# Optimization experiments

Measured on AMD Instinct MI355X. Metric: run time of the kernel, lower is better.

Reference implementation:

```python
import jax, jax.numpy as jnp
import numpy as np

S = 128          # spatial grid size per axis
N = 100000       # active voxels
C_IN = 32
C_OUT = 32
FS = 3           # filter size per axis -> 27 offsets


def _build_rulebook():
    """Build submanifold-conv rulebook: for each active site and each of the
    27 filter offsets, the index of the active neighbor (or masked out)."""
    rng = np.random.default_rng(0)
    coords = rng.integers(0, S, size=(2 * N, 3))
    lin = coords[:, 0] * S * S + coords[:, 1] * S + coords[:, 2]
    lin = np.unique(lin)[:N]                      # sorted unique active sites
    xyz = np.stack([lin // (S * S), (lin // S) % S, lin % S], axis=1)  # [N,3]
    offs = np.stack(np.meshgrid(*([np.arange(FS) - FS // 2] * 3), indexing='ij'), -1).reshape(-1, 3)  # [27,3]
    nb = xyz[:, None, :] + offs[None, :, :]       # [N,27,3]
    inb = np.all((nb >= 0) & (nb < S), axis=-1)   # in-bounds
    nb_lin = nb[..., 0] * S * S + nb[..., 1] * S + nb[..., 2]
    pos = np.searchsorted(lin, nb_lin)
    pos_c = np.clip(pos, 0, N - 1)
    found = inb & (lin[pos_c] == nb_lin)
    nbr_idx = np.where(found, pos_c, 0).astype(np.int32)   # [N,27]
    return nbr_idx, found


def setup_inputs() -> dict:
    key = jax.random.key(0)
    k1, k2 = jax.random.split(key)
    nbr_idx, nbr_mask = _build_rulebook()
    K = FS ** 3
    std = (2.0 / C_IN / K) ** 0.5   # matches module init
    return {
        'features': jax.random.normal(k1, (N, C_IN), dtype=jnp.float32),
        'weight': std * jax.random.normal(k2, (K, C_IN, C_OUT), dtype=jnp.float32),
        'bias': jnp.zeros((C_OUT,), dtype=jnp.float32),
        'nbr_idx': jnp.asarray(nbr_idx),
        'nbr_mask': jnp.asarray(nbr_mask),
    }


def reference(features, weight, bias, nbr_idx, nbr_mask):
    # Submanifold sparse conv: gather active neighbors per filter offset,
    # multiply by per-offset [Cin,Cout] weight, accumulate at active sites.
    gathered = jnp.where(nbr_mask[:, :, None], features[nbr_idx], 0.0)  # [N,K,Cin]
    out = jnp.einsum('nki,kio->no', gathered, weight) + bias            # [N,Cout]
    return out
```

## Files before the change

### kernel.cpp

```cpp
#include <hip/hip_runtime.h>
#include <hip/hip_bf16.h>

#define NVOX 100000
#define CIN 32
#define COUT 32
#define KOFF 27
#define NTILE 6250
#define SENTE (NVOX << 6)

typedef __attribute__((ext_vector_type(8))) short short8;
typedef __attribute__((ext_vector_type(4))) float float4v;
typedef __attribute__((ext_vector_type(4))) int   int4v;

__device__ __forceinline__ short f2bf(float x) {
    union { float f; unsigned u; } v; v.f = x;
    unsigned u = v.u;
    u += 0x7FFFu + ((u >> 16) & 1u);
    return (short)(u >> 16);
}

#define FEAT_BLOCKS 3126

__global__ __launch_bounds__(256) void cvt_kernel(
    const float* __restrict__ feat, const float* __restrict__ weight,
    unsigned short* __restrict__ fbf, short8* __restrict__ wfrag)
{
    if (blockIdx.x < FEAT_BLOCKS) {
        int i = (blockIdx.x * 256 + threadIdx.x) * 4;
        if (i < NVOX * CIN) {
            float4v f = *(const float4v*)(feat + i);
            short s[4] = { f2bf(f.x), f2bf(f.y), f2bf(f.z), f2bf(f.w) };
            *(ulonglong1*)(fbf + i) = *(ulonglong1*)s;
        } else if (i < (NVOX + 1) * CIN) {
            short s[4] = { 0, 0, 0, 0 };
            *(ulonglong1*)(fbf + i) = *(ulonglong1*)s;
        }
    } else {
        int g = (blockIdx.x - FEAT_BLOCKS) * 256 + threadIdx.x;
        if (g >= KOFF * 2 * 64) return;
        int k   = g >> 7;
        int rem = g & 127;
        int t   = rem >> 6;
        int ln  = rem & 63;
        int co  = t * 16 + (ln & 15);
        int cib = (ln >> 4) * 8;
        const float* wp = weight + (k * CIN + cib) * COUT + co;
        short8 b;
#pragma unroll
        for (int j = 0; j < 8; ++j) b[j] = f2bf(wp[j * COUT]);
        wfrag[g] = b;
    }
}

__global__ __launch_bounds__(512, 4) void subm_conv_kernel(
    const unsigned short* __restrict__ fbf,
    const short8* __restrict__ wfrag,
    const float* __restrict__ bias,
    const int* __restrict__ nbr_idx,
    const int* __restrict__ nbr_mask,
    float* __restrict__ out)
{
    __shared__ short8 wlds[KOFF * 2 * 64];

    const int tid  = threadIdx.x;
    const int lane = tid & 63;
    const int wave = tid >> 6;
    const int m    = lane & 15;
    const int quad = lane >> 4;
    const int tile0 = blockIdx.x * 8 + wave;
    const bool tv  = tile0 < NTILE;
    const int tile = tv ? tile0 : (NTILE - 1);
    const int v0   = tile * 16;

    int* meta = (int*)wlds + wave * 448;
    {
        const int tb = v0 * KOFF;
        const int j0 = lane * 4;
        int4v ia = *(const int4v*)(nbr_idx  + tb + j0);
        int4v ma = *(const int4v*)(nbr_mask + tb + j0);
#pragma unroll
        for (int c = 0; c < 4; ++c) {
            int j = j0 + c;
            meta[(j / 27) * 28 + (j % 27)] = (ma[c] ? ia[c] : NVOX) << 6;
        }
        if (j0 < 176) {
            int4v ib = *(const int4v*)(nbr_idx  + tb + 256 + j0);
            int4v mb = *(const int4v*)(nbr_mask + tb + 256 + j0);
#pragma unroll
            for (int c = 0; c < 4; ++c) {
                int j = 256 + j0 + c;
                meta[(j / 27) * 28 + (j % 27)] = (mb[c] ? ib[c] : NVOX) << 6;
            }
        }
    }

    int enc[28];
    {
        const int4v* mp = (const int4v*)(meta + m * 28);
#pragma unroll
        for (int i = 0; i < 7; ++i) {
            int4v t = mp[i];
            enc[i * 4 + 0] = t.x; enc[i * 4 + 1] = t.y;
            enc[i * 4 + 2] = t.z; enc[i * 4 + 3] = t.w;
        }
    }

    unsigned bmv = 0;
#pragma unroll
    for (int k = 0; k < KOFF; ++k)
        bmv |= (__any(enc[k] != SENTE) ? 1u : 0u) << k;
    const unsigned bm = (unsigned)__builtin_amdgcn_readfirstlane((int)bmv);

    __syncthreads();
    for (int g = tid; g < KOFF * 2 * 64; g += 512) wlds[g] = wfrag[g];
    __syncthreads();

    float4v acc0 = {0.f, 0.f, 0.f, 0.f};
    float4v acc1 = {0.f, 0.f, 0.f, 0.f};

    const char* fb   = (const char*)fbf;
    const int   boff = quad * 16;

    short8 abuf[8];
#pragma unroll
    for (int k = 0; k < 8; ++k)
        abuf[k] = *(const short8*)(fb + (size_t)(unsigned)enc[k] + boff);

#pragma unroll
    for (int k = 0; k < KOFF; ++k) {
        const int slot = k & 7;
        short8 a = abuf[slot];
        if (k + 8 < KOFF)
            abuf[slot] = *(const short8*)(fb + (size_t)(unsigned)enc[k + 8] + boff);

        if (bm & (1u << k)) {
            short8 wb0 = wlds[k * 128 + lane];
            short8 wb1 = wlds[k * 128 + 64 + lane];
            acc0 = __builtin_amdgcn_mfma_f32_16x16x32_bf16(a, wb0, acc0, 0, 0, 0);
            acc1 = __builtin_amdgcn_mfma_f32_16x16x32_bf16(a, wb1, acc1, 0, 0, 0);
        }
    }

    __syncthreads();
    float* tb = (float*)wlds + wave * (16 * 36);

    const float bs0 = bias[m];
    const float bs1 = bias[16 + m];
    if (tv) {
#pragma unroll
        for (int r = 0; r < 4; ++r) {
            tb[(quad * 4 + r) * 36 + m]      = acc0[r] + bs0;
            tb[(quad * 4 + r) * 36 + 16 + m] = acc1[r] + bs1;
        }
#pragma unroll
        for (int p = 0; p < 2; ++p) {
            int flat = p * 64 + lane;
            int row  = flat >> 3;
            int ch   = flat & 7;
            float4v val = *(const float4v*)(tb + row * 36 + ch * 4);
            *(float4v*)(out + (size_t)(v0 + row) * COUT + ch * 4) = val;
        }
    }
}

extern "C" void kernel_launch(void* const* d_in, const int* in_sizes, int n_in,
                              void* d_out, int out_size, void* d_ws, size_t ws_size,
                              hipStream_t stream) {
    const float* feat = (const float*)d_in[0];
    const float* wgt  = (const float*)d_in[1];
    const float* bias = (const float*)d_in[2];
    const int*   nidx = (const int*)d_in[3];
    const int*   nmsk = (const int*)d_in[4];
    float*       out  = (float*)d_out;

    char* ws = (char*)d_ws;
    unsigned short* fbf   = (unsigned short*)ws;
    short8*         wfrag = (short8*)(ws + 6400128);

    const int wgt_blocks = (KOFF * 2 * 64 + 255) / 256;
    cvt_kernel<<<FEAT_BLOCKS + wgt_blocks, 256, 0, stream>>>(feat, wgt, fbf, wfrag);

    const int block = 512;
    const int grid  = (NTILE + 7) / 8;
    subm_conv_kernel<<<grid, block, 0, stream>>>(fbf, wfrag, bias, nidx, nmsk, out);
}
```

Measured before the change: 98.96 us.

## Overlap weight staging with metadata loads, swizzle blocks across XCDs, use nontemporal memory ops

The weight fragments are now prefetched into registers at kernel start and written to LDS only after the rulebook metadata is processed. The first feature gathers are also issued before the barrier, so global loads overlap instead of being serialized. Metadata gets its own LDS buffer, which removes one barrier and lets the output staging reuse that buffer. Block IDs are remapped so that contiguous tiles stay on the same XCD, and the rulebook loads and output stores are marked nontemporal. The extra LDS and registers may reduce occupancy.

```diff
diff --git a/kernel.cpp b/kernel.cpp
--- a/kernel.cpp
+++ b/kernel.cpp
@@ -61,31 +61,45 @@
     float* __restrict__ out)
 {
     __shared__ short8 wlds[KOFF * 2 * 64];
+    __shared__ int    mstore[8 * 576];
 
     const int tid  = threadIdx.x;
     const int lane = tid & 63;
     const int wave = tid >> 6;
     const int m    = lane & 15;
     const int quad = lane >> 4;
-    const int tile0 = blockIdx.x * 8 + wave;
-    const bool tv  = tile0 < NTILE;
-    const int tile = tv ? tile0 : (NTILE - 1);
-    const int v0   = tile * 16;
-
-    int* meta = (int*)wlds + wave * 448;
+
+    const int bid  = blockIdx.x;
+    const int xcd  = bid & 7;
+    const int bi   = bid >> 3;
+    const int bswz = (xcd < 6) ? xcd * 98 + bi : 588 + (xcd - 6) * 97 + bi;
+
+    const int tile0 = bswz * 8 + wave;
+    const bool tv   = tile0 < NTILE;
+    const int tile  = tv ? tile0 : (NTILE - 1);
+    const int v0    = tile * 16;
+
+    short8 wreg[7];
+#pragma unroll
+    for (int u = 0; u < 7; ++u) {
+        int g = tid + u * 512;
+        if (g < KOFF * 2 * 64) wreg[u] = wfrag[g];
+    }
+
+    int* meta = mstore + wave * 576;
     {
         const int tb = v0 * KOFF;
         const int j0 = lane * 4;
-        int4v ia = *(const int4v*)(nbr_idx  + tb + j0);
-        int4v ma = *(const int4v*)(nbr_mask + tb + j0);
+        int4v ia = __builtin_nontemporal_load((const int4v*)(nbr_idx  + tb + j0));
+        int4v ma = __builtin_nontemporal_load((const int4v*)(nbr_mask + tb + j0));
 #pragma unroll
         for (int c = 0; c < 4; ++c) {
             int j = j0 + c;
             meta[(j / 27) * 28 + (j % 27)] = (ma[c] ? ia[c] : NVOX) << 6;
         }
         if (j0 < 176) {
-            int4v ib = *(const int4v*)(nbr_idx  + tb + 256 + j0);
-            int4v mb = *(const int4v*)(nbr_mask + tb + 256 + j0);
+            int4v ib = __builtin_nontemporal_load((const int4v*)(nbr_idx  + tb + 256 + j0));
+            int4v mb = __builtin_nontemporal_load((const int4v*)(nbr_mask + tb + 256 + j0));
 #pragma unroll
             for (int c = 0; c < 4; ++c) {
                 int j = 256 + j0 + c;
@@ -111,20 +125,24 @@
         bmv |= (__any(enc[k] != SENTE) ? 1u : 0u) << k;
     const unsigned bm = (unsigned)__builtin_amdgcn_readfirstlane((int)bmv);
 
-    __syncthreads();
-    for (int g = tid; g < KOFF * 2 * 64; g += 512) wlds[g] = wfrag[g];
+#pragma unroll
+    for (int u = 0; u < 7; ++u) {
+        int g = tid + u * 512;
+        if (g < KOFF * 2 * 64) wlds[g] = wreg[u];
+    }
+
+    const char* fb   = (const char*)fbf;
+    const int   boff = quad * 16;
+
+    short8 abuf[8];
+#pragma unroll
+    for (int k = 0; k < 8; ++k)
+        abuf[k] = *(const short8*)(fb + (size_t)(unsigned)enc[k] + boff);
+
     __syncthreads();
 
     float4v acc0 = {0.f, 0.f, 0.f, 0.f};
     float4v acc1 = {0.f, 0.f, 0.f, 0.f};
-
-    const char* fb   = (const char*)fbf;
-    const int   boff = quad * 16;
-
-    short8 abuf[8];
-#pragma unroll
-    for (int k = 0; k < 8; ++k)
-        abuf[k] = *(const short8*)(fb + (size_t)(unsigned)enc[k] + boff);
 
 #pragma unroll
     for (int k = 0; k < KOFF; ++k) {
@@ -141,8 +159,7 @@
         }
     }
 
-    __syncthreads();
-    float* tb = (float*)wlds + wave * (16 * 36);
+    float* tb = (float*)(mstore + wave * 576);
 
     const float bs0 = bias[m];
     const float bs1 = bias[16 + m];
@@ -158,7 +175,7 @@
             int row  = flat >> 3;
             int ch   = flat & 7;
             float4v val = *(const float4v*)(tb + row * 36 + ch * 4);
-            *(float4v*)(out + (size_t)(v0 + row) * COUT + ch * 4) = val;
+            __builtin_nontemporal_store(val, (float4v*)(out + (size_t)(v0 + row) * COUT + ch * 4));
         }
     }
 }
```

Result: no change. 98.49 us (median of 2 runs) (-0.5%).
